# Kernel optimization log

Hardware: AMD Instinct MI355X
Metric: run time of the kernel (lower is better)

## Reference

```python
import jax, jax.numpy as jnp
import numpy as np

HEADS = 16
DIM_HEAD = 64
SCALE = DIM_HEAD ** -0.5


def setup_inputs() -> dict:
    key = jax.random.key(0)
    k1, k2, k3, k4 = jax.random.split(key, 4)
    b, n, dim = 2, 2048, 1024
    inner = HEADS * DIM_HEAD  # 1024
    return {
        "x": jax.random.normal(k1, (b, n, dim), dtype=jnp.float32),
        "x1": jax.random.normal(k2, (b, n, dim), dtype=jnp.float32),
        "W_qkv": jax.random.normal(k3, (dim, inner * 3), dtype=jnp.float32) * (dim ** -0.5),
        "W_out": jax.random.normal(k4, (inner, dim), dtype=jnp.float32) * (inner ** -0.5),
        "b_out": jnp.zeros((dim,), dtype=jnp.float32),
    }


def _split_heads(t):
    b, n, hd = t.shape
    return t.reshape(b, n, HEADS, DIM_HEAD).transpose(0, 2, 1, 3)  # b h n d


def _merge_heads(t):
    b, h, n, d = t.shape
    return t.transpose(0, 2, 1, 3).reshape(b, n, h * d)


def reference(x, x1, W_qkv, W_out, b_out):
    qkv = jnp.split(x @ W_qkv, 3, axis=-1)
    qkv1 = jnp.split(x1 @ W_qkv, 3, axis=-1)
    q, k, v = map(_split_heads, qkv)
    q1, k1, v1 = map(_split_heads, qkv1)

    # cross attention: x queries attend to x1 keys/values, and vice versa
    attn = jax.nn.softmax(jnp.einsum('bhnd,bhmd->bhnm', q, k1) * SCALE, axis=-1)
    attn1 = jax.nn.softmax(jnp.einsum('bhnd,bhmd->bhnm', q1, k) * SCALE, axis=-1)
    out = _merge_heads(jnp.einsum('bhnm,bhmd->bhnd', attn, v1))
    out1 = _merge_heads(jnp.einsum('bhnm,bhmd->bhnd', attn1, v))

    out = out @ W_out + b_out
    out1 = out1 @ W_out + b_out
    return out, out1
```

## Files before the change

kernel.cpp:

```cpp
#include <hip/hip_runtime.h>
#include <hip/hip_bf16.h>


typedef __attribute__((ext_vector_type(8))) short short8;
typedef __attribute__((ext_vector_type(4))) float f32x4;
typedef __attribute__((ext_vector_type(16))) float f32x16;

#define MFMA_BF16(a, b, c) __builtin_amdgcn_mfma_f32_16x16x32_bf16((a), (b), (c), 0, 0, 0)
#define MFMA32(a, b, c)    __builtin_amdgcn_mfma_f32_32x32x16_bf16((a), (b), (c), 0, 0, 0)

__device__ __forceinline__ ushort f2bf(float f) {
    __hip_bfloat16 h = __float2bfloat16(f);
    return *reinterpret_cast<ushort*>(&h);
}

__device__ __forceinline__ unsigned cvtpk(float lo, float hi) {
    unsigned r;
    asm("v_cvt_pk_bf16_f32 %0, %1, %2" : "=v"(r) : "v"(lo), "v"(hi));
    return r;
}

__device__ __forceinline__ void gload_lds16(const void* g, void* l) {
    __builtin_amdgcn_global_load_lds(
        (const __attribute__((address_space(1))) void*)g,
        (__attribute__((address_space(3))) void*)l, 16, 0, 0);
}

__global__ __launch_bounds__(256) void prep_k(const float* __restrict__ x,
                                              const float* __restrict__ x1,
                                              ushort* __restrict__ xb,
                                              const float* __restrict__ wqkv,
                                              ushort* __restrict__ wqkv_t,
                                              const float* __restrict__ wout,
                                              ushort* __restrict__ wout_t) {
    __shared__ ushort tile[32][33];
    const int b = blockIdx.x;
    if (b < 8192) {
        const int idx = b * 256 + threadIdx.x;
        const int half = 1048576;
        const float* src = (idx < half) ? x : x1;
        const int i = (idx < half ? idx : idx - half) * 4;
        float4 v = *(const float4*)(src + i);
        ushort4 o;
        o.x = f2bf(v.x); o.y = f2bf(v.y); o.z = f2bf(v.z); o.w = f2bf(v.w);
        *(ushort4*)(xb + (size_t)idx * 4) = o;
        return;
    }
    const int id = b - 8192;
    int bx = id & 127;
    const int by = id >> 7;
    const float* in; ushort* out; int C;
    if (bx < 96) { in = wqkv; out = wqkv_t; C = 3072; }
    else         { bx -= 96; in = wout; out = wout_t; C = 1024; }
    const int R = 1024;
    const int c0 = bx * 32, r0 = by * 32;
    const int tx = threadIdx.x & 31, ty = threadIdx.x >> 5;
#pragma unroll
    for (int i = 0; i < 4; ++i)
        tile[ty * 4 + i][tx] = f2bf(in[(size_t)(r0 + ty * 4 + i) * C + c0 + tx]);
    __syncthreads();
#pragma unroll
    for (int i = 0; i < 4; ++i)
        out[(size_t)(c0 + ty * 4 + i) * R + r0 + tx] = tile[tx][ty * 4 + i];
}

__global__ __launch_bounds__(256) void qkv_gemm(const ushort* __restrict__ xb,
                                                const ushort* __restrict__ wt,
                                                ushort* __restrict__ qb,
                                                ushort* __restrict__ kb,
                                                ushort* __restrict__ vb) {
    __shared__ __align__(16) ushort Sm[2][128 * 64];
    ushort* As = &Sm[0][0];
    ushort* Bs = &Sm[1][0];

    const int id = blockIdx.x;
    const int xcd = id & 7, j = id >> 3;
    const int nx = xcd * 3 + (j % 3);
    const int n0 = nx * 128;
    const int m0 = (j / 3) * 128;

    const int t = threadIdx.x;
    const int lane = t & 63, w = t >> 6;
    const int wm = (w >> 1) * 64, wn = (w & 1) * 64;
    const int l16 = lane & 15, lq = lane >> 4;

    const int srow = lane >> 3;
    const int scol = ((lane & 7) * 16) ^ (srow << 4);

    f32x4 acc[4][4] = {};

    for (int k0 = 0; k0 < 1024; k0 += 64) {
        __syncthreads();
#pragma unroll
        for (int c = 0; c < 4; ++c) {
            const int ch = w * 4 + c;
            const int row = ch * 8 + srow;
            gload_lds16((const char*)xb + ((size_t)(m0 + row) * 1024 + k0) * 2 + scol,
                        (char*)As + ch * 1024);
            gload_lds16((const char*)wt + ((size_t)(n0 + row) * 1024 + k0) * 2 + scol,
                        (char*)Bs + ch * 1024);
        }
        __syncthreads();
#pragma unroll
        for (int kc = 0; kc < 2; ++kc) {
            short8 a[4], b[4];
#pragma unroll
            for (int i = 0; i < 4; ++i) {
                const int row = wm + i * 16 + l16;
                a[i] = *(const short8*)((const char*)As + row * 128 +
                                        ((kc * 64 + lq * 16) ^ ((row & 7) << 4)));
            }
#pragma unroll
            for (int j2 = 0; j2 < 4; ++j2) {
                const int row = wn + j2 * 16 + l16;
                b[j2] = *(const short8*)((const char*)Bs + row * 128 +
                                         ((kc * 64 + lq * 16) ^ ((row & 7) << 4)));
            }
#pragma unroll
            for (int i = 0; i < 4; ++i)
#pragma unroll
                for (int j2 = 0; j2 < 4; ++j2) acc[i][j2] = MFMA_BF16(a[i], b[j2], acc[i][j2]);
        }
    }

    const int which = (n0 >> 10);

    if (which == 2) {
        __syncthreads();
        char* Cs = (char*)&Sm[0][0];
#pragma unroll
        for (int i = 0; i < 4; ++i)
#pragma unroll
            for (int jj = 0; jj < 4; ++jj) {
                const int ncl = wn + jj * 16 + l16;
                const int mb  = (wm + i * 16 + lq * 4) * 2;
                uint2 pk;
                pk.x = cvtpk(acc[i][jj][0], acc[i][jj][1]);
                pk.y = cvtpk(acc[i][jj][2], acc[i][jj][3]);
                *(uint2*)(Cs + ncl * 256 + (mb ^ ((ncl & 7) << 4))) = pk;
            }
        asm volatile("s_waitcnt lgkmcnt(0)" ::: "memory");
#pragma unroll
        for (int it = 0; it < 8; ++it) {
            const int r  = wn + it * 8 + (lane >> 3);
            const int cb = wm * 2 + (lane & 7) * 16;
            short8 v = *(const short8*)(Cs + r * 256 + (cb ^ ((r & 7) << 4)));
            const int rem = (n0 + r) & 1023;
            const int hh = rem >> 6, d = rem & 63;
            const int m = m0 + wm + (lane & 7) * 8;
            const int ss = m >> 12, mm = m & 4095;
            const int sbv = (ss << 1) | (mm >> 11), pos = mm & 2047;
            *(short8*)(vb + ((size_t)(sbv * 16 + hh) * 64 + d) * 2048 + pos) = v;
        }
        return;
    }

    const float qscale = (which == 0) ? 0.125f : 1.0f;
#pragma unroll
    for (int i = 0; i < 4; ++i) {
#pragma unroll
        for (int jj = 0; jj < 4; ++jj) {
#pragma unroll
            for (int rr = 0; rr < 4; ++rr) {
                const int m = m0 + wm + i * 16 + lq * 4 + rr;
                const int nc = n0 + wn + jj * 16 + l16;
                const ushort bv = f2bf(acc[i][jj][rr] * qscale);
                const int s = m >> 12;
                const int mm = m & 4095;
                const int rem = nc & 1023;
                const int h = rem >> 6, d = rem & 63;
                const int sb = (s << 1) | (mm >> 11);
                const int pos = mm & 2047;
                const size_t bh = (size_t)(sb * 16 + h);
                if (which == 0) qb[(bh * 2048 + pos) * 64 + d] = bv;
                else            kb[(bh * 2048 + pos) * 64 + d] = bv;
            }
        }
    }
}

__global__ __launch_bounds__(256, 4) void attn_k(const ushort* __restrict__ qb,
                                                 const ushort* __restrict__ kb,
                                                 const ushort* __restrict__ vb,
                                                 ushort* __restrict__ ob) {
    __shared__ __align__(16) ushort Ks[2][4096];
    __shared__ __align__(16) ushort Vs[2][4096];

    const int t = threadIdx.x, lane = t & 63, w = t >> 6;
    const int l31 = lane & 31, hi = lane >> 5;

    const int lid = blockIdx.x;
    const int xcd = lid & 7, kk = lid >> 3;
    const int qt = kk & 15;
    const int g = xcd + ((kk >> 4) << 3);
    const int h = g & 15, sb = g >> 4;
    const int s = sb >> 1, bb = sb & 1;
    const int kvsb = ((1 - s) << 1) | bb;
    const int q0 = qt * 128 + w * 32;

    const ushort* qp = qb + (size_t)(sb * 16 + h) * 2048 * 64;
    const char* kp = (const char*)(kb + (size_t)(kvsb * 16 + h) * 2048 * 64);
    const char* vp = (const char*)(vb + (size_t)(kvsb * 16 + h) * 64 * 2048);

    short8 qf[4];
#pragma unroll
    for (int c = 0; c < 4; ++c)
        qf[c] = *(const short8*)(qp + (size_t)(q0 + l31) * 64 + c * 16 + hi * 8);

    f32x16 o0 = {}, o1 = {};
    float lsum = 0.f;

    const int swl = ((lane >> 3) & 7) << 4;
    auto stage = [&](int buf, int key0) {
#pragma unroll
        for (int i = 0; i < 2; ++i) {
            const int ch = w * 2 + i;
            const int off = ch * 1024 + lane * 16;
            gload_lds16(kp + (size_t)key0 * 128 + (off ^ swl),
                        (char*)&Ks[buf][0] + ch * 1024);
            const int rd = ch * 8 + (lane >> 3);
            const int cb = (lane & 7) * 16;
            gload_lds16(vp + (size_t)rd * 4096 + (size_t)key0 * 2 + (cb ^ swl),
                        (char*)&Vs[buf][0] + ch * 1024);
        }
    };

    stage(0, 0);
    __syncthreads();

    const int pl = (l31 & ~12) | ((l31 & 4) << 1) | ((l31 & 8) >> 1);
    const int swp = (pl & 7) << 4;
    const int swv = (l31 & 7) << 4;

    for (int tt = 0; tt < 32; ++tt) {
        const int cur = tt & 1;
        if (tt < 31) stage(cur ^ 1, (tt + 1) * 64);

        const char* Kc = (const char*)&Ks[cur][0];
        const char* Vc = (const char*)&Vs[cur][0];

        f32x16 scA = {}, scB = {};
        __builtin_amdgcn_s_setprio(1);
#pragma unroll
        for (int c = 0; c < 4; ++c) {
            const int off = c * 32 + hi * 16;
            short8 ka  = *(const short8*)(Kc + pl * 128 + (off ^ swp));
            short8 kb2 = *(const short8*)(Kc + (32 + pl) * 128 + (off ^ swp));
            scA = MFMA32(ka, qf[c], scA);
            scB = MFMA32(kb2, qf[c], scB);
        }
        __builtin_amdgcn_s_setprio(0);

#pragma unroll
        for (int r = 0; r < 16; ++r) scA[r] = __expf(scA[r]);
#pragma unroll
        for (int r = 0; r < 16; ++r) scB[r] = __expf(scB[r]);
        {
            float sA = (((scA[0] + scA[1]) + (scA[2] + scA[3])) +
                        ((scA[4] + scA[5]) + (scA[6] + scA[7]))) +
                       (((scA[8] + scA[9]) + (scA[10] + scA[11])) +
                        ((scA[12] + scA[13]) + (scA[14] + scA[15])));
            float sB = (((scB[0] + scB[1]) + (scB[2] + scB[3])) +
                        ((scB[4] + scB[5]) + (scB[6] + scB[7]))) +
                       (((scB[8] + scB[9]) + (scB[10] + scB[11])) +
                        ((scB[12] + scB[13]) + (scB[14] + scB[15])));
            lsum += sA + sB;
        }

        __builtin_amdgcn_s_setprio(1);
#define PACK_PV(P, BASE, KS)                                                     \
        {                                                                        \
            union { unsigned u[4]; short8 s8; } ap;                              \
            ap.u[0] = cvtpk(P[BASE + 0], P[BASE + 1]);                           \
            ap.u[1] = cvtpk(P[BASE + 2], P[BASE + 3]);                           \
            ap.u[2] = cvtpk(P[BASE + 4], P[BASE + 5]);                           \
            ap.u[3] = cvtpk(P[BASE + 6], P[BASE + 7]);                           \
            const int vo = (KS) * 32 + hi * 16;                                  \
            short8 v0 = *(const short8*)(Vc + l31 * 128 + (vo ^ swv));           \
            short8 v1 = *(const short8*)(Vc + (32 + l31) * 128 + (vo ^ swv));    \
            o0 = MFMA32(ap.s8, v0, o0);                                          \
            o1 = MFMA32(ap.s8, v1, o1);                                          \
        }
        PACK_PV(scA, 0, 0)
        PACK_PV(scA, 8, 1)
        PACK_PV(scB, 0, 2)
        PACK_PV(scB, 8, 3)
#undef PACK_PV
        __builtin_amdgcn_s_setprio(0);

        __syncthreads();
    }

    const float lf = lsum + __shfl_xor(lsum, 32);
    const size_t obase = (size_t)(sb * 2048 + q0) * 1024 + h * 64 + l31;
#pragma unroll
    for (int r = 0; r < 16; ++r) {
        const int qrow = (r & 3) + 8 * (r >> 2) + 4 * hi;
        const float invl = 1.f / __shfl(lf, qrow);
        ob[obase + (size_t)qrow * 1024]      = f2bf(o0[r] * invl);
        ob[obase + (size_t)qrow * 1024 + 32] = f2bf(o1[r] * invl);
    }
}

__global__ __launch_bounds__(256) void out_gemm(const ushort* __restrict__ ob,
                                                const ushort* __restrict__ wot,
                                                const float* __restrict__ bias,
                                                float* __restrict__ out) {
    __shared__ __align__(16) ushort As[128 * 64];
    __shared__ __align__(16) ushort Bs[128 * 64];

    const int n0 = blockIdx.x * 128;
    const int m0 = blockIdx.y * 128;
    const int t = threadIdx.x;
    const int lane = t & 63, w = t >> 6;
    const int wm = (w >> 1) * 64, wn = (w & 1) * 64;
    const int l16 = lane & 15, lq = lane >> 4;

    const int srow = lane >> 3;
    const int scol = ((lane & 7) * 16) ^ (srow << 4);

    f32x4 acc[4][4] = {};

    for (int k0 = 0; k0 < 1024; k0 += 64) {
        __syncthreads();
#pragma unroll
        for (int c = 0; c < 4; ++c) {
            const int ch = w * 4 + c;
            const int row = ch * 8 + srow;
            gload_lds16((const char*)ob + ((size_t)(m0 + row) * 1024 + k0) * 2 + scol,
                        (char*)As + ch * 1024);
            gload_lds16((const char*)wot + ((size_t)(n0 + row) * 1024 + k0) * 2 + scol,
                        (char*)Bs + ch * 1024);
        }
        __syncthreads();
#pragma unroll
        for (int kc = 0; kc < 2; ++kc) {
            short8 a[4], b[4];
#pragma unroll
            for (int i = 0; i < 4; ++i) {
                const int row = wm + i * 16 + l16;
                a[i] = *(const short8*)((const char*)As + row * 128 +
                                        ((kc * 64 + lq * 16) ^ ((row & 7) << 4)));
            }
#pragma unroll
            for (int j = 0; j < 4; ++j) {
                const int row = wn + j * 16 + l16;
                b[j] = *(const short8*)((const char*)Bs + row * 128 +
                                        ((kc * 64 + lq * 16) ^ ((row & 7) << 4)));
            }
#pragma unroll
            for (int i = 0; i < 4; ++i)
#pragma unroll
                for (int j = 0; j < 4; ++j) acc[i][j] = MFMA_BF16(a[i], b[j], acc[i][j]);
        }
    }

    float biasf[4];
#pragma unroll
    for (int jj = 0; jj < 4; ++jj) biasf[jj] = bias[n0 + wn + jj * 16 + l16];

#pragma unroll
    for (int i = 0; i < 4; ++i)
#pragma unroll
        for (int jj = 0; jj < 4; ++jj)
#pragma unroll
            for (int rr = 0; rr < 4; ++rr) {
                const int m = m0 + wm + i * 16 + lq * 4 + rr;
                const int nc = n0 + wn + jj * 16 + l16;
                out[(size_t)m * 1024 + nc] = acc[i][jj][rr] + biasf[jj];
            }
}

extern "C" void kernel_launch(void* const* d_in, const int* in_sizes, int n_in,
                              void* d_out, int out_size, void* d_ws, size_t ws_size,
                              hipStream_t stream) {
    (void)out_size; (void)ws_size;
    const float *x = nullptr, *x1 = nullptr, *wqkv = nullptr, *wout = nullptr, *bias = nullptr;
    for (int i = 0; i < n_in; ++i) {
        const int sz = in_sizes[i];
        const float* p = (const float*)d_in[i];
        if (sz == 4194304)      { if (!x) x = p; else x1 = p; }
        else if (sz == 3145728) wqkv = p;
        else if (sz == 1048576) wout = p;
        else if (sz == 1024)    bias = p;
    }
    float* out = (float*)d_out;

    ushort* ws      = (ushort*)d_ws;
    ushort* wqkv_t  = ws;
    ushort* wout_t  = wqkv_t + 3072 * 1024;
    ushort* xb      = wout_t + 1024 * 1024;
    ushort* qbuf    = xb + 8388608;
    ushort* kbuf    = qbuf + 8388608;
    ushort* vbuf    = kbuf + 8388608;
    ushort* obuf    = xb;

    prep_k<<<12288, 256, 0, stream>>>(x, x1, xb, wqkv, wqkv_t, wout, wout_t);
    qkv_gemm<<<1536, 256, 0, stream>>>(xb, wqkv_t, qbuf, kbuf, vbuf);
    attn_k<<<1024, 256, 0, stream>>>(qbuf, kbuf, vbuf, obuf);
    out_gemm<<<dim3(8, 64), 256, 0, stream>>>(obuf, wout_t, bias, out);
}
```

Before: 275.3 us.

## Triple-buffer K/V staging with one barrier and compute row sums via MFMA

The attention kernel moves from double to triple buffering of K/V tiles in LDS. It now waits on an explicit vmcnt and uses a single barrier per iteration, so loads run two tiles ahead and the trailing __syncthreads is gone. The softmax denominator is now accumulated by an extra MFMA against a ones vector instead of a scalar add tree and cross-lane shuffles, which also rounds P to bf16 consistently with the PV product. LDS use grows and occupancy bounds drop from 4 to 3 blocks per CU, and each iteration now issues 12 MFMAs instead of 8.

```diff
diff --git a/kernel.cpp b/kernel.cpp
--- a/kernel.cpp
+++ b/kernel.cpp
@@ -179,12 +179,12 @@
     }
 }
 
-__global__ __launch_bounds__(256, 4) void attn_k(const ushort* __restrict__ qb,
+__global__ __launch_bounds__(256, 3) void attn_k(const ushort* __restrict__ qb,
                                                  const ushort* __restrict__ kb,
                                                  const ushort* __restrict__ vb,
                                                  ushort* __restrict__ ob) {
-    __shared__ __align__(16) ushort Ks[2][4096];
-    __shared__ __align__(16) ushort Vs[2][4096];
+    __shared__ __align__(16) ushort Ks[3][4096];
+    __shared__ __align__(16) ushort Vs[3][4096];
 
     const int t = threadIdx.x, lane = t & 63, w = t >> 6;
     const int l31 = lane & 31, hi = lane >> 5;
@@ -207,8 +207,12 @@
     for (int c = 0; c < 4; ++c)
         qf[c] = *(const short8*)(qp + (size_t)(q0 + l31) * 64 + c * 16 + hi * 8);
 
+    short8 ones;
+#pragma unroll
+    for (int j = 0; j < 8; ++j) ones[j] = (short)0x3F80;
+
     f32x16 o0 = {}, o1 = {};
-    float lsum = 0.f;
+    f32x16 l_acc = {};
 
     const int swl = ((lane >> 3) & 7) << 4;
     auto stage = [&](int buf, int key0) {
@@ -226,15 +230,21 @@
     };
 
     stage(0, 0);
-    __syncthreads();
+    stage(1, 64);
 
     const int pl = (l31 & ~12) | ((l31 & 4) << 1) | ((l31 & 8) >> 1);
     const int swp = (pl & 7) << 4;
     const int swv = (l31 & 7) << 4;
 
+    int cur = 0;
     for (int tt = 0; tt < 32; ++tt) {
-        const int cur = tt & 1;
-        if (tt < 31) stage(cur ^ 1, (tt + 1) * 64);
+        if (tt < 31) asm volatile("s_waitcnt vmcnt(4)" ::: "memory");
+        else         asm volatile("s_waitcnt vmcnt(0)" ::: "memory");
+        __builtin_amdgcn_s_barrier();
+        if (tt < 30) {
+            int nb = cur + 2; if (nb >= 3) nb -= 3;
+            stage(nb, (tt + 2) * 64);
+        }
 
         const char* Kc = (const char*)&Ks[cur][0];
         const char* Vc = (const char*)&Vs[cur][0];
@@ -255,17 +265,6 @@
         for (int r = 0; r < 16; ++r) scA[r] = __expf(scA[r]);
 #pragma unroll
         for (int r = 0; r < 16; ++r) scB[r] = __expf(scB[r]);
-        {
-            float sA = (((scA[0] + scA[1]) + (scA[2] + scA[3])) +
-                        ((scA[4] + scA[5]) + (scA[6] + scA[7]))) +
-                       (((scA[8] + scA[9]) + (scA[10] + scA[11])) +
-                        ((scA[12] + scA[13]) + (scA[14] + scA[15])));
-            float sB = (((scB[0] + scB[1]) + (scB[2] + scB[3])) +
-                        ((scB[4] + scB[5]) + (scB[6] + scB[7]))) +
-                       (((scB[8] + scB[9]) + (scB[10] + scB[11])) +
-                        ((scB[12] + scB[13]) + (scB[14] + scB[15])));
-            lsum += sA + sB;
-        }
 
         __builtin_amdgcn_s_setprio(1);
 #define PACK_PV(P, BASE, KS)                                                     \
@@ -280,6 +279,7 @@
             short8 v1 = *(const short8*)(Vc + (32 + l31) * 128 + (vo ^ swv));    \
             o0 = MFMA32(ap.s8, v0, o0);                                          \
             o1 = MFMA32(ap.s8, v1, o1);                                          \
+            l_acc = MFMA32(ap.s8, ones, l_acc);                                  \
         }
         PACK_PV(scA, 0, 0)
         PACK_PV(scA, 8, 1)
@@ -288,15 +288,14 @@
 #undef PACK_PV
         __builtin_amdgcn_s_setprio(0);
 
-        __syncthreads();
-    }
-
-    const float lf = lsum + __shfl_xor(lsum, 32);
+        cur = (cur == 2) ? 0 : cur + 1;
+    }
+
     const size_t obase = (size_t)(sb * 2048 + q0) * 1024 + h * 64 + l31;
 #pragma unroll
     for (int r = 0; r < 16; ++r) {
         const int qrow = (r & 3) + 8 * (r >> 2) + 4 * hi;
-        const float invl = 1.f / __shfl(lf, qrow);
+        const float invl = 1.f / l_acc[r];
         ob[obase + (size_t)qrow * 1024]      = f2bf(o0[r] * invl);
         ob[obase + (size_t)qrow * 1024 + 32] = f2bf(o1[r] * invl);
     }
```

Result: no change. 278.9 us (+1.3%).
